# Kernel optimization log

Hardware: AMD Instinct MI355X
Metric: run time of the kernel (lower is better)

The kernel has to match this reference:

```python
import jax, jax.numpy as jnp
import numpy as np

NUM_TOKENS = 2048
NUM_HEADS = 32
NUM_KV_HEADS = 8
HEAD_DIM = 128
ATTN_SCALE = 0.08838834764831845  # 1/sqrt(head_dim)


def setup_inputs() -> dict:
    key = jax.random.key(0)
    kq, kk, kv = jax.random.split(key, 3)
    q = jax.random.normal(kq, (NUM_TOKENS, NUM_HEADS, HEAD_DIM), dtype=jnp.float32)
    k = jax.random.normal(kk, (NUM_TOKENS, NUM_KV_HEADS, HEAD_DIM), dtype=jnp.float32)
    v = jax.random.normal(kv, (NUM_TOKENS, NUM_KV_HEADS, HEAD_DIM), dtype=jnp.float32)
    return {"q": q, "k": k, "v": v}


def reference(q, k, v):
    # Prefill path: all tokens attend causally; GQA expands kv heads.
    n_rep = NUM_HEADS // NUM_KV_HEADS
    k = jnp.repeat(k, n_rep, axis=1)  # (T, H, D)
    v = jnp.repeat(v, n_rep, axis=1)  # (T, H, D)
    # scores: (H, Tq, Tk)
    scores = jnp.einsum("thd,shd->hts", q, k) * ATTN_SCALE
    T = q.shape[0]
    causal = jnp.tril(jnp.ones((T, T), dtype=bool))  # (Tq, Tk)
    scores = jnp.where(causal[None, :, :], scores, -jnp.inf)
    weights = jax.nn.softmax(scores, axis=-1)
    out = jnp.einsum("hts,shd->thd", weights, v)  # (T, H, D)
    return out
```

## Files before the change

kernel.cpp:

```cpp
#include <hip/hip_runtime.h>

#define NT 2048
#define NH 32
#define NKV 8
#define HD 128
#define BM 128
#define BN 64
#define BN2 128
#define NQT (NT / BM)
#define SCALE_LOG2E 0.12754984003389239f
#define NEG_BIG -1.0e30f

typedef unsigned int   uint4v  __attribute__((ext_vector_type(4)));
typedef float          f32x4   __attribute__((ext_vector_type(4)));
typedef __bf16         bf16x8  __attribute__((ext_vector_type(8)));
typedef unsigned short u16;

#define KIMG 8192
#define VIMG 8192
#define KT128 16384
#define VT128 16384

__device__ __forceinline__ unsigned f2bf(float f) {
  return (__builtin_bit_cast(unsigned, f) + 0x8000u) >> 16;
}
__device__ __forceinline__ unsigned pack_rn(float lo, float hi) {
  const unsigned ul = __builtin_bit_cast(unsigned, lo) + 0x8000u;
  const unsigned uh = __builtin_bit_cast(unsigned, hi) + 0x8000u;
  return __builtin_amdgcn_perm(ul, uh, 0x03020706u);
}

__device__ __forceinline__ void gload16(const u16* g, u16* l) {
  __builtin_amdgcn_global_load_lds(
      (const __attribute__((address_space(1))) unsigned int*)g,
      (__attribute__((address_space(3))) unsigned int*)l, 16, 0, 0);
}

__global__ __launch_bounds__(256, 2)
void prep_kernel(const float* __restrict__ kg, const float* __restrict__ vg,
                 u16* __restrict__ wsk, u16* __restrict__ wsv) {
  __shared__ __align__(16) float lds_f[64 * 132];
  const int tid = threadIdx.x;
  const int hk  = (int)blockIdx.x >> 5;
  const int t   = (int)blockIdx.x & 31;
  const int kv0 = t * 64;
  u16* __restrict__ kimg = wsk + (size_t)(hk * 32 + t) * KIMG;
  u16* __restrict__ vimg = wsv + (size_t)(hk * 16 + (t >> 1)) * VT128;
  const int half = t & 1;

#pragma unroll
  for (int it = 0; it < 4; ++it) {
    const int unit = it * 256 + tid;
    const int kv = unit >> 4, ch = unit & 15;
    const float* kp = &kg[((kv0 + kv) * NKV + hk) * HD + ch * 8];
    const f32x4 a = *(const f32x4*)kp;
    const f32x4 b = *(const f32x4*)(kp + 4);
    uint4v pk;
    pk[0] = pack_rn(a[0], a[1]);
    pk[1] = pack_rn(a[2], a[3]);
    pk[2] = pack_rn(b[0], b[1]);
    pk[3] = pack_rn(b[2], b[3]);
    *(uint4v*)&kimg[kv * 128 + ((ch * 8) ^ ((kv & 7) << 3))] = pk;
  }

#pragma unroll
  for (int it = 0; it < 8; ++it) {
    const int unit = it * 256 + tid;
    const int kv = unit >> 5, c4 = unit & 31;
    *(f32x4*)&lds_f[kv * 132 + c4 * 4] =
        *(const f32x4*)&vg[((kv0 + kv) * NKV + hk) * HD + c4 * 4];
  }
  __syncthreads();

#pragma unroll
  for (int it = 0; it < 4; ++it) {
    const int unit = it * 256 + tid;
    const int d = unit >> 3, chunk = unit & 7;
    const int c2 = chunk >> 2, qd = chunk & 3;
    const int kb = c2 * 32 + qd * 4;
    uint4v w;
    w[0] = pack_rn(lds_f[(kb + 0) * 132 + d],  lds_f[(kb + 1) * 132 + d]);
    w[1] = pack_rn(lds_f[(kb + 2) * 132 + d],  lds_f[(kb + 3) * 132 + d]);
    w[2] = pack_rn(lds_f[(kb + 16) * 132 + d], lds_f[(kb + 17) * 132 + d]);
    w[3] = pack_rn(lds_f[(kb + 18) * 132 + d], lds_f[(kb + 19) * 132 + d]);
    *(uint4v*)&vimg[d * 128 + (((half * 8 + chunk) * 8) ^ ((d & 7) << 3))] = w;
  }
}

__global__ __launch_bounds__(512, 2)
void fa2_kernel(const float* __restrict__ qg, float* __restrict__ og,
                const u16* __restrict__ wsk, const u16* __restrict__ wsv) {
  __shared__ __align__(16) u16 lds[2][KT128 + VT128];

  const int tid  = threadIdx.x;
  const int lane = tid & 63;
  const int w    = tid >> 6;
  const int rg   = w & 3;
  const int g    = w >> 2;
  const int quad = lane >> 4;
  const int l16  = lane & 15;

  const int n = (int)blockIdx.x;
  const int x = n & 31;
  const int h  = ((x & 7) << 2) | (x >> 3);
  const int hk = h >> 2;
  const int qt = (NQT - 1) - (n >> 5);
  const int q0  = qt * BM;
  const int q0w = q0 + rg * 32;
  const int njt = qt + 1;

  uint4v qf[2][4];
#pragma unroll
  for (int qn = 0; qn < 2; ++qn)
#pragma unroll
    for (int c = 0; c < 4; ++c) {
      const int row = q0w + qn * 16 + l16;
      const float* qp = &qg[(row * NH + h) * HD + c * 32 + quad * 8];
      const f32x4 a = *(const f32x4*)qp;
      const f32x4 b = *(const f32x4*)(qp + 4);
      uint4v rgv;
      rgv[0] = pack_rn(a[0] * SCALE_LOG2E, a[1] * SCALE_LOG2E);
      rgv[1] = pack_rn(a[2] * SCALE_LOG2E, a[3] * SCALE_LOG2E);
      rgv[2] = pack_rn(b[0] * SCALE_LOG2E, b[1] * SCALE_LOG2E);
      rgv[3] = pack_rn(b[2] * SCALE_LOG2E, b[3] * SCALE_LOG2E);
      qf[qn][c] = rgv;
    }

  f32x4 o[8][2];
#pragma unroll
  for (int nt = 0; nt < 8; ++nt)
#pragma unroll
    for (int qn = 0; qn < 2; ++qn)
#pragma unroll
      for (int r = 0; r < 4; ++r) o[nt][qn][r] = 0.f;

  float l_run[2] = {0.f, 0.f};

  int kro[4], vro[2];
#pragma unroll
  for (int c = 0; c < 4; ++c)
    kro[c] = l16 * 128 + ((c * 32 + quad * 8) ^ ((l16 & 7) << 3));
#pragma unroll
  for (int c2 = 0; c2 < 2; ++c2)
    vro[c2] = l16 * 128 + ((((g * 2 + c2) * 4 + quad) * 8) ^ ((l16 & 7) << 3));

  const int lkbase = g * 8192;

  auto stage_dma = [&](int jt, int bb) {
    const u16* ks = wsk + (size_t)(hk * 32 + jt * 2) * KIMG;
    const u16* vs = wsv + (size_t)(hk * 16 + jt) * VT128;
#pragma unroll
    for (int r = 0; r < 4; ++r) {
      const int fl = r * 512 + tid;
      gload16(ks + fl * 8, &lds[bb][fl * 8]);
    }
#pragma unroll
    for (int r = 0; r < 4; ++r) {
      const int fl = r * 512 + tid;
      gload16(vs + fl * 8, &lds[bb][KT128 + fl * 8]);
    }
  };

  stage_dma(0, 0);
  __asm__ __volatile__("s_waitcnt vmcnt(0)" ::: "memory");
  __syncthreads();

  for (int jt = 0; jt < njt; ++jt) {
    const int kv0g = jt * BN2 + g * 64;
    const int b    = jt & 1;
    const bool havenext = (jt + 1 < njt);

    if (havenext) stage_dma(jt + 1, b ^ 1);

    if (kv0g <= q0w + 31) {
      const u16* lk = &lds[b][lkbase];
      const u16* lv = &lds[b][KT128];

      f32x4 s[4][2];
#pragma unroll
      for (int mt = 0; mt < 4; ++mt)
#pragma unroll
        for (int qn = 0; qn < 2; ++qn)
#pragma unroll
          for (int r = 0; r < 4; ++r) s[mt][qn][r] = 0.f;

      __builtin_amdgcn_s_setprio(1);
#pragma unroll
      for (int c = 0; c < 4; ++c) {
#pragma unroll
        for (int mt = 0; mt < 4; ++mt) {
          const uint4v kf = *(const uint4v*)&lk[mt * 2048 + kro[c]];
#pragma unroll
          for (int qn = 0; qn < 2; ++qn)
            s[mt][qn] = __builtin_amdgcn_mfma_f32_16x16x32_bf16(
                __builtin_bit_cast(bf16x8, kf),
                __builtin_bit_cast(bf16x8, qf[qn][c]), s[mt][qn], 0, 0, 0);
        }
      }
      __builtin_amdgcn_s_setprio(0);

      if (kv0g + 63 > q0w) {
#pragma unroll
        for (int mt = 0; mt < 4; ++mt)
#pragma unroll
          for (int qn = 0; qn < 2; ++qn)
#pragma unroll
            for (int r = 0; r < 4; ++r) {
              const int kvgl = kv0g + mt * 16 + quad * 4 + r;
              const int qgl  = q0w + qn * 16 + l16;
              if (kvgl > qgl) s[mt][qn][r] = NEG_BIG;
            }
      }

      unsigned pk[4][2][2];
#pragma unroll
      for (int qn = 0; qn < 2; ++qn) {
        float ts = 0.f;
#pragma unroll
        for (int mt = 0; mt < 4; ++mt) {
#pragma unroll
          for (int r = 0; r < 4; ++r) {
            const float p = __builtin_amdgcn_exp2f(s[mt][qn][r]);
            s[mt][qn][r] = p;
            ts += p;
          }
          pk[mt][qn][0] = pack_rn(s[mt][qn][0], s[mt][qn][1]);
          pk[mt][qn][1] = pack_rn(s[mt][qn][2], s[mt][qn][3]);
        }
        l_run[qn] += ts;
      }

      __builtin_amdgcn_s_setprio(1);
#pragma unroll
      for (int c2 = 0; c2 < 2; ++c2) {
        uint4v pf[2];
#pragma unroll
        for (int qn = 0; qn < 2; ++qn) {
          pf[qn][0] = pk[2 * c2][qn][0];
          pf[qn][1] = pk[2 * c2][qn][1];
          pf[qn][2] = pk[2 * c2 + 1][qn][0];
          pf[qn][3] = pk[2 * c2 + 1][qn][1];
        }
#pragma unroll
        for (int nt = 0; nt < 8; ++nt) {
          const uint4v vf = *(const uint4v*)&lv[nt * 2048 + vro[c2]];
#pragma unroll
          for (int qn = 0; qn < 2; ++qn)
            o[nt][qn] = __builtin_amdgcn_mfma_f32_16x16x32_bf16(
                __builtin_bit_cast(bf16x8, vf),
                __builtin_bit_cast(bf16x8, pf[qn]), o[nt][qn], 0, 0, 0);
        }
      }
      __builtin_amdgcn_s_setprio(0);
    }

    if (havenext) {
      __asm__ __volatile__("s_waitcnt vmcnt(0)" ::: "memory");
      __syncthreads();
    }
  }

  float li[2];
#pragma unroll
  for (int qn = 0; qn < 2; ++qn) {
    float l = l_run[qn];
    l += __shfl_xor(l, 16);
    l += __shfl_xor(l, 32);
    li[qn] = l;
  }

  __syncthreads();
  float* red  = (float*)&lds[0][0];
  float* lred = red + 128 * 132;
  if (g == 1) {
#pragma unroll
    for (int qn = 0; qn < 2; ++qn) {
      const int q = rg * 32 + qn * 16 + l16;
      if (quad == 0) lred[q] = li[qn];
#pragma unroll
      for (int nt = 0; nt < 8; ++nt)
        *(f32x4*)&red[q * 132 + nt * 16 + quad * 4] = o[nt][qn];
    }
  }
  __syncthreads();
  if (g == 0) {
#pragma unroll
    for (int qn = 0; qn < 2; ++qn) {
      const int q = rg * 32 + qn * 16 + l16;
      const float inv = 1.0f / (li[qn] + lred[q]);
      float* orow = &og[((q0 + q) * NH + h) * HD + quad * 4];
#pragma unroll
      for (int nt = 0; nt < 8; ++nt) {
        const f32x4 op = *(const f32x4*)&red[q * 132 + nt * 16 + quad * 4];
        f32x4 ov;
#pragma unroll
        for (int r = 0; r < 4; ++r) ov[r] = (o[nt][qn][r] + op[r]) * inv;
        *(f32x4*)(orow + nt * 16) = ov;
      }
    }
  }
}

__global__ __launch_bounds__(256, 2)
void fa_raw(const float* __restrict__ qg, const float* __restrict__ kg,
            const float* __restrict__ vg, float* __restrict__ og) {
  __shared__ __align__(16) u16 lds[2][KIMG + VIMG];

  const int tid  = threadIdx.x;
  const int lane = tid & 63;
  const int w    = tid >> 6;
  const int quad = lane >> 4;
  const int l16  = lane & 15;

  const int h  = (int)blockIdx.x;
  const int hk = h >> 2;
  const int y  = (int)blockIdx.y;
  const int qt = (y < NQT / 2) ? (NQT - 1 - y) : (y - NQT / 2);
  const int q0  = qt * BM;
  const int q0w = q0 + w * 32;

  uint4v qf[2][4];
#pragma unroll
  for (int qn = 0; qn < 2; ++qn)
#pragma unroll
    for (int c = 0; c < 4; ++c) {
      const int row = q0w + qn * 16 + l16;
      const float* qp = &qg[(row * NH + h) * HD + c * 32 + quad * 8];
      const f32x4 a = *(const f32x4*)qp;
      const f32x4 b = *(const f32x4*)(qp + 4);
      uint4v rg;
      rg[0] = pack_rn(a[0] * SCALE_LOG2E, a[1] * SCALE_LOG2E);
      rg[1] = pack_rn(a[2] * SCALE_LOG2E, a[3] * SCALE_LOG2E);
      rg[2] = pack_rn(b[0] * SCALE_LOG2E, b[1] * SCALE_LOG2E);
      rg[3] = pack_rn(b[2] * SCALE_LOG2E, b[3] * SCALE_LOG2E);
      qf[qn][c] = rg;
    }

  f32x4 o[8][2];
#pragma unroll
  for (int nt = 0; nt < 8; ++nt)
#pragma unroll
    for (int qn = 0; qn < 2; ++qn)
#pragma unroll
      for (int r = 0; r < 4; ++r) o[nt][qn][r] = 0.f;
  float l_run[2] = {0.f, 0.f};

  const int njt = 2 * qt + 2;

  int kro[4], vro[2];
#pragma unroll
  for (int c = 0; c < 4; ++c)
    kro[c] = l16 * 128 + ((c * 32 + quad * 8) ^ ((l16 & 7) << 3));
#pragma unroll
  for (int c2 = 0; c2 < 2; ++c2)
    vro[c2] = l16 * 64 + ((c2 * 32 + quad * 8) ^ ((l16 & 7) << 3));

  const int posl = (lane >> 5) * 32 + (((lane & 15) >> 2) << 3) +
                   (((lane >> 4) & 1) << 2) + (lane & 3);

  f32x4 kregf[4][2], vregf[4][2];

  auto stage_load_f = [&](int jt) {
    const int kvb = jt * BN;
#pragma unroll
    for (int r = 0; r < 4; ++r) {
      const int flat = r * 256 + tid;
      const float* kp = &kg[((kvb + (flat >> 4)) * NKV + hk) * HD + (flat & 15) * 8];
      kregf[r][0] = *(const f32x4*)kp;
      kregf[r][1] = *(const f32x4*)(kp + 4);
    }
#pragma unroll
    for (int r = 0; r < 4; ++r) {
      const int d0 = (r * 4 + w) * 8;
      const float* vp = &vg[((kvb + lane) * NKV + hk) * HD + d0];
      vregf[r][0] = *(const f32x4*)vp;
      vregf[r][1] = *(const f32x4*)(vp + 4);
    }
  };
  auto stage_write_f = [&](int bb) {
#pragma unroll
    for (int r = 0; r < 4; ++r) {
      const int flat = r * 256 + tid;
      const int kv = flat >> 4, ch = flat & 15;
      uint4v pk;
      pk[0] = pack_rn(kregf[r][0][0], kregf[r][0][1]);
      pk[1] = pack_rn(kregf[r][0][2], kregf[r][0][3]);
      pk[2] = pack_rn(kregf[r][1][0], kregf[r][1][1]);
      pk[3] = pack_rn(kregf[r][1][2], kregf[r][1][3]);
      *(uint4v*)&lds[bb][kv * 128 + ((ch * 8) ^ ((kv & 7) << 3))] = pk;
    }
#pragma unroll
    for (int r = 0; r < 4; ++r) {
      const int d0 = (r * 4 + w) * 8;
#pragma unroll
      for (int e = 0; e < 8; ++e) {
        const int d = d0 + e;
        const float val = (e < 4) ? vregf[r][0][e] : vregf[r][1][e - 4];
        lds[bb][KIMG + d * 64 + (posl ^ ((d & 7) << 3))] = (u16)f2bf(val);
      }
    }
  };

  stage_load_f(0);
  stage_write_f(0);
  __syncthreads();

  for (int jt = 0; jt < njt; ++jt) {
    const int kv0 = jt * BN;
    const int b   = jt & 1;
    const bool havenext = (jt + 1 < njt);
    if (havenext) stage_load_f(jt + 1);

    if (kv0 <= q0w + 31) {
      const u16* lk = &lds[b][0];
      const u16* lv = &lds[b][KIMG];

      f32x4 s[4][2];
#pragma unroll
      for (int mt = 0; mt < 4; ++mt)
#pragma unroll
        for (int qn = 0; qn < 2; ++qn)
#pragma unroll
          for (int r = 0; r < 4; ++r) s[mt][qn][r] = 0.f;

#pragma unroll
      for (int c = 0; c < 4; ++c)
#pragma unroll
        for (int mt = 0; mt < 4; ++mt) {
          const uint4v kf = *(const uint4v*)&lk[mt * 2048 + kro[c]];
#pragma unroll
          for (int qn = 0; qn < 2; ++qn)
            s[mt][qn] = __builtin_amdgcn_mfma_f32_16x16x32_bf16(
                __builtin_bit_cast(bf16x8, kf),
                __builtin_bit_cast(bf16x8, qf[qn][c]), s[mt][qn], 0, 0, 0);
        }

      if (kv0 + BN - 1 > q0w) {
#pragma unroll
        for (int mt = 0; mt < 4; ++mt)
#pragma unroll
          for (int qn = 0; qn < 2; ++qn)
#pragma unroll
            for (int r = 0; r < 4; ++r) {
              const int kvgl = kv0 + mt * 16 + quad * 4 + r;
              const int qgl  = q0w + qn * 16 + l16;
              if (kvgl > qgl) s[mt][qn][r] = NEG_BIG;
            }
      }

      unsigned pk[4][2][2];
#pragma unroll
      for (int qn = 0; qn < 2; ++qn) {
        float ts = 0.f;
#pragma unroll
        for (int mt = 0; mt < 4; ++mt) {
#pragma unroll
          for (int r = 0; r < 4; ++r) {
            const float p = __builtin_amdgcn_exp2f(s[mt][qn][r]);
            s[mt][qn][r] = p;
            ts += p;
          }
          pk[mt][qn][0] = pack_rn(s[mt][qn][0], s[mt][qn][1]);
          pk[mt][qn][1] = pack_rn(s[mt][qn][2], s[mt][qn][3]);
        }
        l_run[qn] += ts;
      }

#pragma unroll
      for (int c2 = 0; c2 < 2; ++c2) {
        uint4v pf[2];
#pragma unroll
        for (int qn = 0; qn < 2; ++qn) {
          pf[qn][0] = pk[2 * c2][qn][0];
          pf[qn][1] = pk[2 * c2][qn][1];
          pf[qn][2] = pk[2 * c2 + 1][qn][0];
          pf[qn][3] = pk[2 * c2 + 1][qn][1];
        }
#pragma unroll
        for (int nt = 0; nt < 8; ++nt) {
          const uint4v vf = *(const uint4v*)&lv[nt * 1024 + vro[c2]];
#pragma unroll
          for (int qn = 0; qn < 2; ++qn)
            o[nt][qn] = __builtin_amdgcn_mfma_f32_16x16x32_bf16(
                __builtin_bit_cast(bf16x8, vf),
                __builtin_bit_cast(bf16x8, pf[qn]), o[nt][qn], 0, 0, 0);
        }
      }
    }

    if (havenext) {
      stage_write_f(b ^ 1);
      __syncthreads();
    }
  }

#pragma unroll
  for (int qn = 0; qn < 2; ++qn) {
    float l = l_run[qn];
    l += __shfl_xor(l, 16);
    l += __shfl_xor(l, 32);
    const float inv = 1.0f / l;
    float* orow = &og[((q0w + qn * 16 + l16) * NH + h) * HD + quad * 4];
#pragma unroll
    for (int nt = 0; nt < 8; ++nt) {
      f32x4 ov;
#pragma unroll
      for (int r = 0; r < 4; ++r) ov[r] = o[nt][qn][r] * inv;
      *(f32x4*)(orow + nt * 16) = ov;
    }
  }
}

extern "C" void kernel_launch(void* const* d_in, const int* in_sizes, int n_in,
                              void* d_out, int out_size, void* d_ws, size_t ws_size,
                              hipStream_t stream) {
  (void)in_sizes; (void)n_in; (void)out_size;
  const float* q = (const float*)d_in[0];
  const float* k = (const float*)d_in[1];
  const float* v = (const float*)d_in[2];
  float* out = (float*)d_out;

  const size_t kv_bytes = (size_t)NKV * NT * HD * 2;
  if (ws_size >= 2 * kv_bytes) {
    u16* wsk = (u16*)d_ws;
    u16* wsv = wsk + (size_t)NKV * NT * HD;
    prep_kernel<<<dim3(NKV * 32), dim3(256), 0, stream>>>(k, v, wsk, wsv);
    fa2_kernel<<<dim3(NH * NQT), dim3(512), 0, stream>>>(q, out, wsk, wsv);
  } else {
    fa_raw<<<dim3(NH, NQT), dim3(256), 0, stream>>>(q, k, v, out);
  }
}
```

Before: 138.3 us.

## Software-pipeline QK of tile j with softmax/PV of tile j-1

Restructures the main loop so each iteration computes QK^T scores for the current KV tile while doing the exp, pack and PV MFMAs for the previous tile. Score registers ping-pong between two buffers, and K and V loads are staged separately, with V loaded one iteration later than K. The aim is to let exp/VALU work overlap MFMA work and to hide load latency better. The cost is higher register pressure from two score tiles, which may reduce occupancy or cause spills, plus an epilogue step.

New measurement: 139.7 us. Within noise of the previous version (+1.0%).

```diff
diff --git a/kernel.cpp b/kernel.cpp
--- a/kernel.cpp
+++ b/kernel.cpp
@@ -146,117 +146,136 @@
 
   const int lkbase = g * 8192;
 
-  auto stage_dma = [&](int jt, int bb) {
+  auto stage_k = [&](int jt) {
     const u16* ks = wsk + (size_t)(hk * 32 + jt * 2) * KIMG;
-    const u16* vs = wsv + (size_t)(hk * 16 + jt) * VT128;
+    u16* dst = &lds[jt & 1][0];
 #pragma unroll
     for (int r = 0; r < 4; ++r) {
       const int fl = r * 512 + tid;
-      gload16(ks + fl * 8, &lds[bb][fl * 8]);
-    }
+      gload16(ks + fl * 8, dst + fl * 8);
+    }
+  };
+  auto stage_v = [&](int jt) {
+    const u16* vs = wsv + (size_t)(hk * 16 + jt) * VT128;
+    u16* dst = &lds[jt & 1][KT128];
 #pragma unroll
     for (int r = 0; r < 4; ++r) {
       const int fl = r * 512 + tid;
-      gload16(vs + fl * 8, &lds[bb][KT128 + fl * 8]);
-    }
-  };
-
-  stage_dma(0, 0);
+      gload16(vs + fl * 8, dst + fl * 8);
+    }
+  };
+
+  auto qk_step = [&](int b, f32x4 (&S)[4][2]) {
+    const u16* lk = &lds[b][lkbase];
+#pragma unroll
+    for (int mt = 0; mt < 4; ++mt)
+#pragma unroll
+      for (int qn = 0; qn < 2; ++qn)
+#pragma unroll
+        for (int r = 0; r < 4; ++r) S[mt][qn][r] = 0.f;
+    __builtin_amdgcn_s_setprio(1);
+#pragma unroll
+    for (int c = 0; c < 4; ++c) {
+#pragma unroll
+      for (int mt = 0; mt < 4; ++mt) {
+        const uint4v kf = *(const uint4v*)&lk[mt * 2048 + kro[c]];
+#pragma unroll
+        for (int qn = 0; qn < 2; ++qn)
+          S[mt][qn] = __builtin_amdgcn_mfma_f32_16x16x32_bf16(
+              __builtin_bit_cast(bf16x8, kf),
+              __builtin_bit_cast(bf16x8, qf[qn][c]), S[mt][qn], 0, 0, 0);
+      }
+    }
+    __builtin_amdgcn_s_setprio(0);
+  };
+
+  auto smpv_step = [&](int kv0p, int bp, f32x4 (&S)[4][2]) {
+    if (kv0p + 63 > q0w) {
+#pragma unroll
+      for (int mt = 0; mt < 4; ++mt)
+#pragma unroll
+        for (int qn = 0; qn < 2; ++qn)
+#pragma unroll
+          for (int r = 0; r < 4; ++r) {
+            const int kvgl = kv0p + mt * 16 + quad * 4 + r;
+            const int qgl  = q0w + qn * 16 + l16;
+            if (kvgl > qgl) S[mt][qn][r] = NEG_BIG;
+          }
+    }
+    unsigned pk[4][2][2];
+#pragma unroll
+    for (int qn = 0; qn < 2; ++qn) {
+      float ts = 0.f;
+#pragma unroll
+      for (int mt = 0; mt < 4; ++mt) {
+#pragma unroll
+        for (int r = 0; r < 4; ++r) {
+          const float p = __builtin_amdgcn_exp2f(S[mt][qn][r]);
+          S[mt][qn][r] = p;
+          ts += p;
+        }
+        pk[mt][qn][0] = pack_rn(S[mt][qn][0], S[mt][qn][1]);
+        pk[mt][qn][1] = pack_rn(S[mt][qn][2], S[mt][qn][3]);
+      }
+      l_run[qn] += ts;
+    }
+    const u16* lv = &lds[bp][KT128];
+    __builtin_amdgcn_s_setprio(1);
+#pragma unroll
+    for (int c2 = 0; c2 < 2; ++c2) {
+      uint4v pf[2];
+#pragma unroll
+      for (int qn = 0; qn < 2; ++qn) {
+        pf[qn][0] = pk[2 * c2][qn][0];
+        pf[qn][1] = pk[2 * c2][qn][1];
+        pf[qn][2] = pk[2 * c2 + 1][qn][0];
+        pf[qn][3] = pk[2 * c2 + 1][qn][1];
+      }
+#pragma unroll
+      for (int nt = 0; nt < 8; ++nt) {
+        const uint4v vf = *(const uint4v*)&lv[nt * 2048 + vro[c2]];
+#pragma unroll
+        for (int qn = 0; qn < 2; ++qn)
+          o[nt][qn] = __builtin_amdgcn_mfma_f32_16x16x32_bf16(
+              __builtin_bit_cast(bf16x8, vf),
+              __builtin_bit_cast(bf16x8, pf[qn]), o[nt][qn], 0, 0, 0);
+      }
+    }
+    __builtin_amdgcn_s_setprio(0);
+  };
+
+  f32x4 sA[4][2], sB[4][2];
+
+  auto iter = [&](int jt, f32x4 (&SC)[4][2], f32x4 (&SP)[4][2]) {
+    const int b = jt & 1;
+    const int kv0c = jt * BN2 + g * 64;
+    if (jt + 1 < njt) stage_k(jt + 1);
+    stage_v(jt);
+    if (kv0c <= q0w + 31) qk_step(b, SC);
+    if (jt > 0) {
+      const int kv0p = kv0c - BN2;
+      if (kv0p <= q0w + 31) smpv_step(kv0p, b ^ 1, SP);
+    }
+    __asm__ __volatile__("s_waitcnt vmcnt(0)" ::: "memory");
+    __syncthreads();
+  };
+
+  stage_k(0);
   __asm__ __volatile__("s_waitcnt vmcnt(0)" ::: "memory");
   __syncthreads();
 
-  for (int jt = 0; jt < njt; ++jt) {
-    const int kv0g = jt * BN2 + g * 64;
-    const int b    = jt & 1;
-    const bool havenext = (jt + 1 < njt);
-
-    if (havenext) stage_dma(jt + 1, b ^ 1);
-
-    if (kv0g <= q0w + 31) {
-      const u16* lk = &lds[b][lkbase];
-      const u16* lv = &lds[b][KT128];
-
-      f32x4 s[4][2];
-#pragma unroll
-      for (int mt = 0; mt < 4; ++mt)
-#pragma unroll
-        for (int qn = 0; qn < 2; ++qn)
-#pragma unroll
-          for (int r = 0; r < 4; ++r) s[mt][qn][r] = 0.f;
-
-      __builtin_amdgcn_s_setprio(1);
-#pragma unroll
-      for (int c = 0; c < 4; ++c) {
-#pragma unroll
-        for (int mt = 0; mt < 4; ++mt) {
-          const uint4v kf = *(const uint4v*)&lk[mt * 2048 + kro[c]];
-#pragma unroll
-          for (int qn = 0; qn < 2; ++qn)
-            s[mt][qn] = __builtin_amdgcn_mfma_f32_16x16x32_bf16(
-                __builtin_bit_cast(bf16x8, kf),
-                __builtin_bit_cast(bf16x8, qf[qn][c]), s[mt][qn], 0, 0, 0);
-        }
-      }
-      __builtin_amdgcn_s_setprio(0);
-
-      if (kv0g + 63 > q0w) {
-#pragma unroll
-        for (int mt = 0; mt < 4; ++mt)
-#pragma unroll
-          for (int qn = 0; qn < 2; ++qn)
-#pragma unroll
-            for (int r = 0; r < 4; ++r) {
-              const int kvgl = kv0g + mt * 16 + quad * 4 + r;
-              const int qgl  = q0w + qn * 16 + l16;
-              if (kvgl > qgl) s[mt][qn][r] = NEG_BIG;
-            }
-      }
-
-      unsigned pk[4][2][2];
-#pragma unroll
-      for (int qn = 0; qn < 2; ++qn) {
-        float ts = 0.f;
-#pragma unroll
-        for (int mt = 0; mt < 4; ++mt) {
-#pragma unroll
-          for (int r = 0; r < 4; ++r) {
-            const float p = __builtin_amdgcn_exp2f(s[mt][qn][r]);
-            s[mt][qn][r] = p;
-            ts += p;
-          }
-          pk[mt][qn][0] = pack_rn(s[mt][qn][0], s[mt][qn][1]);
-          pk[mt][qn][1] = pack_rn(s[mt][qn][2], s[mt][qn][3]);
-        }
-        l_run[qn] += ts;
-      }
-
-      __builtin_amdgcn_s_setprio(1);
-#pragma unroll
-      for (int c2 = 0; c2 < 2; ++c2) {
-        uint4v pf[2];
-#pragma unroll
-        for (int qn = 0; qn < 2; ++qn) {
-          pf[qn][0] = pk[2 * c2][qn][0];
-          pf[qn][1] = pk[2 * c2][qn][1];
-          pf[qn][2] = pk[2 * c2 + 1][qn][0];
-          pf[qn][3] = pk[2 * c2 + 1][qn][1];
-        }
-#pragma unroll
-        for (int nt = 0; nt < 8; ++nt) {
-          const uint4v vf = *(const uint4v*)&lv[nt * 2048 + vro[c2]];
-#pragma unroll
-          for (int qn = 0; qn < 2; ++qn)
-            o[nt][qn] = __builtin_amdgcn_mfma_f32_16x16x32_bf16(
-                __builtin_bit_cast(bf16x8, vf),
-                __builtin_bit_cast(bf16x8, pf[qn]), o[nt][qn], 0, 0, 0);
-        }
-      }
-      __builtin_amdgcn_s_setprio(0);
-    }
-
-    if (havenext) {
-      __asm__ __volatile__("s_waitcnt vmcnt(0)" ::: "memory");
-      __syncthreads();
+  int jt = 0;
+  for (; jt + 1 < njt; jt += 2) {
+    iter(jt, sA, sB);
+    iter(jt + 1, sB, sA);
+  }
+  if (jt < njt) iter(jt, sA, sB);
+
+  {
+    const int kv0l = (njt - 1) * BN2 + g * 64;
+    if (kv0l <= q0w + 31) {
+      if ((njt - 1) & 1) smpv_step(kv0l, (njt - 1) & 1, sB);
+      else               smpv_step(kv0l, (njt - 1) & 1, sA);
     }
   }
 
```

## Replace LDS-staged split-KV kernel with direct global-to-register fragment loads

Applied to the files above, without the earlier changes.

The 512-thread kernel is replaced by a 256-thread kernel. It drops LDS double buffering and the two-group KV split with its LDS reduction. Each wave now loads K and V MFMA fragments straight from the bf16 workspace into registers, relying on the cache for reuse across waves and blocks. The prep kernel writes unswizzled 64-row tiles to match, and q-tiles are paired heavy/light for load balance. This removes LDS traffic and barriers, but it exposes global load latency with no explicit prefetch and raises register pressure.

Result: slower. 211.0 us (+52.5%).

```diff
diff --git a/kernel.cpp b/kernel.cpp
--- a/kernel.cpp
+++ b/kernel.cpp
@@ -6,7 +6,6 @@
 #define HD 128
 #define BM 128
 #define BN 64
-#define BN2 128
 #define NQT (NT / BM)
 #define SCALE_LOG2E 0.12754984003389239f
 #define NEG_BIG -1.0e30f
@@ -18,8 +17,6 @@
 
 #define KIMG 8192
 #define VIMG 8192
-#define KT128 16384
-#define VT128 16384
 
 __device__ __forceinline__ unsigned f2bf(float f) {
   return (__builtin_bit_cast(unsigned, f) + 0x8000u) >> 16;
@@ -28,12 +25,6 @@
   const unsigned ul = __builtin_bit_cast(unsigned, lo) + 0x8000u;
   const unsigned uh = __builtin_bit_cast(unsigned, hi) + 0x8000u;
   return __builtin_amdgcn_perm(ul, uh, 0x03020706u);
-}
-
-__device__ __forceinline__ void gload16(const u16* g, u16* l) {
-  __builtin_amdgcn_global_load_lds(
-      (const __attribute__((address_space(1))) unsigned int*)g,
-      (__attribute__((address_space(3))) unsigned int*)l, 16, 0, 0);
 }
 
 __global__ __launch_bounds__(256, 2)
@@ -45,8 +36,7 @@
   const int t   = (int)blockIdx.x & 31;
   const int kv0 = t * 64;
   u16* __restrict__ kimg = wsk + (size_t)(hk * 32 + t) * KIMG;
-  u16* __restrict__ vimg = wsv + (size_t)(hk * 16 + (t >> 1)) * VT128;
-  const int half = t & 1;
+  u16* __restrict__ vimg = wsv + (size_t)(hk * 32 + t) * VIMG;
 
 #pragma unroll
   for (int it = 0; it < 4; ++it) {
@@ -60,7 +50,7 @@
     pk[1] = pack_rn(a[2], a[3]);
     pk[2] = pack_rn(b[0], b[1]);
     pk[3] = pack_rn(b[2], b[3]);
-    *(uint4v*)&kimg[kv * 128 + ((ch * 8) ^ ((kv & 7) << 3))] = pk;
+    *(uint4v*)&kimg[kv * 128 + ch * 8] = pk;
   }
 
 #pragma unroll
@@ -83,239 +73,25 @@
     w[1] = pack_rn(lds_f[(kb + 2) * 132 + d],  lds_f[(kb + 3) * 132 + d]);
     w[2] = pack_rn(lds_f[(kb + 16) * 132 + d], lds_f[(kb + 17) * 132 + d]);
     w[3] = pack_rn(lds_f[(kb + 18) * 132 + d], lds_f[(kb + 19) * 132 + d]);
-    *(uint4v*)&vimg[d * 128 + (((half * 8 + chunk) * 8) ^ ((d & 7) << 3))] = w;
-  }
-}
-
-__global__ __launch_bounds__(512, 2)
-void fa2_kernel(const float* __restrict__ qg, float* __restrict__ og,
+    *(uint4v*)&vimg[d * 64 + chunk * 8] = w;
+  }
+}
+
+__global__ __launch_bounds__(256, 2)
+void fa3_kernel(const float* __restrict__ qg, float* __restrict__ og,
                 const u16* __restrict__ wsk, const u16* __restrict__ wsv) {
-  __shared__ __align__(16) u16 lds[2][KT128 + VT128];
-
-  const int tid  = threadIdx.x;
-  const int lane = tid & 63;
-  const int w    = tid >> 6;
-  const int rg   = w & 3;
-  const int g    = w >> 2;
-  const int quad = lane >> 4;
-  const int l16  = lane & 15;
-
-  const int n = (int)blockIdx.x;
-  const int x = n & 31;
-  const int h  = ((x & 7) << 2) | (x >> 3);
-  const int hk = h >> 2;
-  const int qt = (NQT - 1) - (n >> 5);
-  const int q0  = qt * BM;
-  const int q0w = q0 + rg * 32;
-  const int njt = qt + 1;
-
-  uint4v qf[2][4];
-#pragma unroll
-  for (int qn = 0; qn < 2; ++qn)
-#pragma unroll
-    for (int c = 0; c < 4; ++c) {
-      const int row = q0w + qn * 16 + l16;
-      const float* qp = &qg[(row * NH + h) * HD + c * 32 + quad * 8];
-      const f32x4 a = *(const f32x4*)qp;
-      const f32x4 b = *(const f32x4*)(qp + 4);
-      uint4v rgv;
-      rgv[0] = pack_rn(a[0] * SCALE_LOG2E, a[1] * SCALE_LOG2E);
-      rgv[1] = pack_rn(a[2] * SCALE_LOG2E, a[3] * SCALE_LOG2E);
-      rgv[2] = pack_rn(b[0] * SCALE_LOG2E, b[1] * SCALE_LOG2E);
-      rgv[3] = pack_rn(b[2] * SCALE_LOG2E, b[3] * SCALE_LOG2E);
-      qf[qn][c] = rgv;
-    }
-
-  f32x4 o[8][2];
-#pragma unroll
-  for (int nt = 0; nt < 8; ++nt)
-#pragma unroll
-    for (int qn = 0; qn < 2; ++qn)
-#pragma unroll
-      for (int r = 0; r < 4; ++r) o[nt][qn][r] = 0.f;
-
-  float l_run[2] = {0.f, 0.f};
-
-  int kro[4], vro[2];
-#pragma unroll
-  for (int c = 0; c < 4; ++c)
-    kro[c] = l16 * 128 + ((c * 32 + quad * 8) ^ ((l16 & 7) << 3));
-#pragma unroll
-  for (int c2 = 0; c2 < 2; ++c2)
-    vro[c2] = l16 * 128 + ((((g * 2 + c2) * 4 + quad) * 8) ^ ((l16 & 7) << 3));
-
-  const int lkbase = g * 8192;
-
-  auto stage_dma = [&](int jt, int bb) {
-    const u16* ks = wsk + (size_t)(hk * 32 + jt * 2) * KIMG;
-    const u16* vs = wsv + (size_t)(hk * 16 + jt) * VT128;
-#pragma unroll
-    for (int r = 0; r < 4; ++r) {
-      const int fl = r * 512 + tid;
-      gload16(ks + fl * 8, &lds[bb][fl * 8]);
-    }
-#pragma unroll
-    for (int r = 0; r < 4; ++r) {
-      const int fl = r * 512 + tid;
-      gload16(vs + fl * 8, &lds[bb][KT128 + fl * 8]);
-    }
-  };
-
-  stage_dma(0, 0);
-  __asm__ __volatile__("s_waitcnt vmcnt(0)" ::: "memory");
-  __syncthreads();
-
-  for (int jt = 0; jt < njt; ++jt) {
-    const int kv0g = jt * BN2 + g * 64;
-    const int b    = jt & 1;
-    const bool havenext = (jt + 1 < njt);
-
-    if (havenext) stage_dma(jt + 1, b ^ 1);
-
-    if (kv0g <= q0w + 31) {
-      const u16* lk = &lds[b][lkbase];
-      const u16* lv = &lds[b][KT128];
-
-      f32x4 s[4][2];
-#pragma unroll
-      for (int mt = 0; mt < 4; ++mt)
-#pragma unroll
-        for (int qn = 0; qn < 2; ++qn)
-#pragma unroll
-          for (int r = 0; r < 4; ++r) s[mt][qn][r] = 0.f;
-
-      __builtin_amdgcn_s_setprio(1);
-#pragma unroll
-      for (int c = 0; c < 4; ++c) {
-#pragma unroll
-        for (int mt = 0; mt < 4; ++mt) {
-          const uint4v kf = *(const uint4v*)&lk[mt * 2048 + kro[c]];
-#pragma unroll
-          for (int qn = 0; qn < 2; ++qn)
-            s[mt][qn] = __builtin_amdgcn_mfma_f32_16x16x32_bf16(
-                __builtin_bit_cast(bf16x8, kf),
-                __builtin_bit_cast(bf16x8, qf[qn][c]), s[mt][qn], 0, 0, 0);
-        }
-      }
-      __builtin_amdgcn_s_setprio(0);
-
-      if (kv0g + 63 > q0w) {
-#pragma unroll
-        for (int mt = 0; mt < 4; ++mt)
-#pragma unroll
-          for (int qn = 0; qn < 2; ++qn)
-#pragma unroll
-            for (int r = 0; r < 4; ++r) {
-              const int kvgl = kv0g + mt * 16 + quad * 4 + r;
-              const int qgl  = q0w + qn * 16 + l16;
-              if (kvgl > qgl) s[mt][qn][r] = NEG_BIG;
-            }
-      }
-
-      unsigned pk[4][2][2];
-#pragma unroll
-      for (int qn = 0; qn < 2; ++qn) {
-        float ts = 0.f;
-#pragma unroll
-        for (int mt = 0; mt < 4; ++mt) {
-#pragma unroll
-          for (int r = 0; r < 4; ++r) {
-            const float p = __builtin_amdgcn_exp2f(s[mt][qn][r]);
-            s[mt][qn][r] = p;
-            ts += p;
-          }
-          pk[mt][qn][0] = pack_rn(s[mt][qn][0], s[mt][qn][1]);
-          pk[mt][qn][1] = pack_rn(s[mt][qn][2], s[mt][qn][3]);
-        }
-        l_run[qn] += ts;
-      }
-
-      __builtin_amdgcn_s_setprio(1);
-#pragma unroll
-      for (int c2 = 0; c2 < 2; ++c2) {
-        uint4v pf[2];
-#pragma unroll
-        for (int qn = 0; qn < 2; ++qn) {
-          pf[qn][0] = pk[2 * c2][qn][0];
-          pf[qn][1] = pk[2 * c2][qn][1];
-          pf[qn][2] = pk[2 * c2 + 1][qn][0];
-          pf[qn][3] = pk[2 * c2 + 1][qn][1];
-        }
-#pragma unroll
-        for (int nt = 0; nt < 8; ++nt) {
-          const uint4v vf = *(const uint4v*)&lv[nt * 2048 + vro[c2]];
-#pragma unroll
-          for (int qn = 0; qn < 2; ++qn)
-            o[nt][qn] = __builtin_amdgcn_mfma_f32_16x16x32_bf16(
-                __builtin_bit_cast(bf16x8, vf),
-                __builtin_bit_cast(bf16x8, pf[qn]), o[nt][qn], 0, 0, 0);
-        }
-      }
-      __builtin_amdgcn_s_setprio(0);
-    }
-
-    if (havenext) {
-      __asm__ __volatile__("s_waitcnt vmcnt(0)" ::: "memory");
-      __syncthreads();
-    }
-  }
-
-  float li[2];
-#pragma unroll
-  for (int qn = 0; qn < 2; ++qn) {
-    float l = l_run[qn];
-    l += __shfl_xor(l, 16);
-    l += __shfl_xor(l, 32);
-    li[qn] = l;
-  }
-
-  __syncthreads();
-  float* red  = (float*)&lds[0][0];
-  float* lred = red + 128 * 132;
-  if (g == 1) {
-#pragma unroll
-    for (int qn = 0; qn < 2; ++qn) {
-      const int q = rg * 32 + qn * 16 + l16;
-      if (quad == 0) lred[q] = li[qn];
-#pragma unroll
-      for (int nt = 0; nt < 8; ++nt)
-        *(f32x4*)&red[q * 132 + nt * 16 + quad * 4] = o[nt][qn];
-    }
-  }
-  __syncthreads();
-  if (g == 0) {
-#pragma unroll
-    for (int qn = 0; qn < 2; ++qn) {
-      const int q = rg * 32 + qn * 16 + l16;
-      const float inv = 1.0f / (li[qn] + lred[q]);
-      float* orow = &og[((q0 + q) * NH + h) * HD + quad * 4];
-#pragma unroll
-      for (int nt = 0; nt < 8; ++nt) {
-        const f32x4 op = *(const f32x4*)&red[q * 132 + nt * 16 + quad * 4];
-        f32x4 ov;
-#pragma unroll
-        for (int r = 0; r < 4; ++r) ov[r] = (o[nt][qn][r] + op[r]) * inv;
-        *(f32x4*)(orow + nt * 16) = ov;
-      }
-    }
-  }
-}
-
-__global__ __launch_bounds__(256, 2)
-void fa_raw(const float* __restrict__ qg, const float* __restrict__ kg,
-            const float* __restrict__ vg, float* __restrict__ og) {
-  __shared__ __align__(16) u16 lds[2][KIMG + VIMG];
-
   const int tid  = threadIdx.x;
   const int lane = tid & 63;
   const int w    = tid >> 6;
   const int quad = lane >> 4;
   const int l16  = lane & 15;
 
-  const int h  = (int)blockIdx.x;
+  const int n = (int)blockIdx.x;
+  const int x = n & 31;
+  const int y = n >> 5;
+  const int h  = ((x & 7) << 2) | (x >> 3);
   const int hk = h >> 2;
-  const int y  = (int)blockIdx.y;
-  const int qt = (y < NQT / 2) ? (NQT - 1 - y) : (y - NQT / 2);
+  const int qt = (y < 8) ? (15 - y) : (y - 8);
   const int q0  = qt * BM;
   const int q0w = q0 + w * 32;
 
@@ -343,6 +119,168 @@
     for (int qn = 0; qn < 2; ++qn)
 #pragma unroll
       for (int r = 0; r < 4; ++r) o[nt][qn][r] = 0.f;
+
+  float l_run[2] = {0.f, 0.f};
+
+  const int koff = l16 * 128 + quad * 8;
+  const int voff = l16 * 64 + quad * 8;
+
+  const u16* kb = wsk + (size_t)hk * 32 * KIMG;
+  const u16* vb = wsv + (size_t)hk * 32 * VIMG;
+
+  const int jlast = (q0w + 31) >> 6;
+
+  for (int jt = 0; jt <= jlast; ++jt) {
+    const int kv0 = jt * BN;
+    const u16* kt = kb + (size_t)jt * KIMG;
+    const u16* vt = vb + (size_t)jt * VIMG;
+
+    uint4v kf[4][4];
+#pragma unroll
+    for (int c = 0; c < 4; ++c)
+#pragma unroll
+      for (int mt = 0; mt < 4; ++mt)
+        kf[c][mt] = *(const uint4v*)&kt[mt * 2048 + c * 32 + koff];
+
+    uint4v vf[2][8];
+#pragma unroll
+    for (int c2 = 0; c2 < 2; ++c2)
+#pragma unroll
+      for (int nt = 0; nt < 8; ++nt)
+        vf[c2][nt] = *(const uint4v*)&vt[nt * 1024 + c2 * 32 + voff];
+
+    f32x4 s[4][2];
+#pragma unroll
+    for (int mt = 0; mt < 4; ++mt)
+#pragma unroll
+      for (int qn = 0; qn < 2; ++qn)
+#pragma unroll
+        for (int r = 0; r < 4; ++r) s[mt][qn][r] = 0.f;
+
+    __builtin_amdgcn_s_setprio(1);
+#pragma unroll
+    for (int c = 0; c < 4; ++c)
+#pragma unroll
+      for (int mt = 0; mt < 4; ++mt)
+#pragma unroll
+        for (int qn = 0; qn < 2; ++qn)
+          s[mt][qn] = __builtin_amdgcn_mfma_f32_16x16x32_bf16(
+              __builtin_bit_cast(bf16x8, kf[c][mt]),
+              __builtin_bit_cast(bf16x8, qf[qn][c]), s[mt][qn], 0, 0, 0);
+    __builtin_amdgcn_s_setprio(0);
+
+    if (kv0 + BN - 1 > q0w) {
+#pragma unroll
+      for (int mt = 0; mt < 4; ++mt)
+#pragma unroll
+        for (int qn = 0; qn < 2; ++qn)
+#pragma unroll
+          for (int r = 0; r < 4; ++r) {
+            const int kvgl = kv0 + mt * 16 + quad * 4 + r;
+            const int qgl  = q0w + qn * 16 + l16;
+            if (kvgl > qgl) s[mt][qn][r] = NEG_BIG;
+          }
+    }
+
+    unsigned pk[4][2][2];
+#pragma unroll
+    for (int qn = 0; qn < 2; ++qn) {
+      float ts = 0.f;
+#pragma unroll
+      for (int mt = 0; mt < 4; ++mt) {
+#pragma unroll
+        for (int r = 0; r < 4; ++r) {
+          const float p = __builtin_amdgcn_exp2f(s[mt][qn][r]);
+          s[mt][qn][r] = p;
+          ts += p;
+        }
+        pk[mt][qn][0] = pack_rn(s[mt][qn][0], s[mt][qn][1]);
+        pk[mt][qn][1] = pack_rn(s[mt][qn][2], s[mt][qn][3]);
+      }
+      l_run[qn] += ts;
+    }
+
+    __builtin_amdgcn_s_setprio(1);
+#pragma unroll
+    for (int c2 = 0; c2 < 2; ++c2) {
+      uint4v pf[2];
+#pragma unroll
+      for (int qn = 0; qn < 2; ++qn) {
+        pf[qn][0] = pk[2 * c2][qn][0];
+        pf[qn][1] = pk[2 * c2][qn][1];
+        pf[qn][2] = pk[2 * c2 + 1][qn][0];
+        pf[qn][3] = pk[2 * c2 + 1][qn][1];
+      }
+#pragma unroll
+      for (int nt = 0; nt < 8; ++nt)
+#pragma unroll
+        for (int qn = 0; qn < 2; ++qn)
+          o[nt][qn] = __builtin_amdgcn_mfma_f32_16x16x32_bf16(
+              __builtin_bit_cast(bf16x8, vf[c2][nt]),
+              __builtin_bit_cast(bf16x8, pf[qn]), o[nt][qn], 0, 0, 0);
+    }
+    __builtin_amdgcn_s_setprio(0);
+  }
+
+#pragma unroll
+  for (int qn = 0; qn < 2; ++qn) {
+    float l = l_run[qn];
+    l += __shfl_xor(l, 16);
+    l += __shfl_xor(l, 32);
+    const float inv = 1.0f / l;
+    float* orow = &og[((q0w + qn * 16 + l16) * NH + h) * HD + quad * 4];
+#pragma unroll
+    for (int nt = 0; nt < 8; ++nt) {
+      f32x4 ov;
+#pragma unroll
+      for (int r = 0; r < 4; ++r) ov[r] = o[nt][qn][r] * inv;
+      *(f32x4*)(orow + nt * 16) = ov;
+    }
+  }
+}
+
+__global__ __launch_bounds__(256, 2)
+void fa_raw(const float* __restrict__ qg, const float* __restrict__ kg,
+            const float* __restrict__ vg, float* __restrict__ og) {
+  __shared__ __align__(16) u16 lds[2][KIMG + VIMG];
+
+  const int tid  = threadIdx.x;
+  const int lane = tid & 63;
+  const int w    = tid >> 6;
+  const int quad = lane >> 4;
+  const int l16  = lane & 15;
+
+  const int h  = (int)blockIdx.x;
+  const int hk = h >> 2;
+  const int y  = (int)blockIdx.y;
+  const int qt = (y < NQT / 2) ? (NQT - 1 - y) : (y - NQT / 2);
+  const int q0  = qt * BM;
+  const int q0w = q0 + w * 32;
+
+  uint4v qf[2][4];
+#pragma unroll
+  for (int qn = 0; qn < 2; ++qn)
+#pragma unroll
+    for (int c = 0; c < 4; ++c) {
+      const int row = q0w + qn * 16 + l16;
+      const float* qp = &qg[(row * NH + h) * HD + c * 32 + quad * 8];
+      const f32x4 a = *(const f32x4*)qp;
+      const f32x4 b = *(const f32x4*)(qp + 4);
+      uint4v rg;
+      rg[0] = pack_rn(a[0] * SCALE_LOG2E, a[1] * SCALE_LOG2E);
+      rg[1] = pack_rn(a[2] * SCALE_LOG2E, a[3] * SCALE_LOG2E);
+      rg[2] = pack_rn(b[0] * SCALE_LOG2E, b[1] * SCALE_LOG2E);
+      rg[3] = pack_rn(b[2] * SCALE_LOG2E, b[3] * SCALE_LOG2E);
+      qf[qn][c] = rg;
+    }
+
+  f32x4 o[8][2];
+#pragma unroll
+  for (int nt = 0; nt < 8; ++nt)
+#pragma unroll
+    for (int qn = 0; qn < 2; ++qn)
+#pragma unroll
+      for (int r = 0; r < 4; ++r) o[nt][qn][r] = 0.f;
   float l_run[2] = {0.f, 0.f};
 
   const int njt = 2 * qt + 2;
@@ -525,7 +463,7 @@
     u16* wsk = (u16*)d_ws;
     u16* wsv = wsk + (size_t)NKV * NT * HD;
     prep_kernel<<<dim3(NKV * 32), dim3(256), 0, stream>>>(k, v, wsk, wsv);
-    fa2_kernel<<<dim3(NH * NQT), dim3(512), 0, stream>>>(q, out, wsk, wsv);
+    fa3_kernel<<<dim3(NH * NQT), dim3(256), 0, stream>>>(q, out, wsk, wsv);
   } else {
     fa_raw<<<dim3(NH, NQT), dim3(256), 0, stream>>>(q, k, v, out);
   }
```
